# Performance work log

Measured on AMD Instinct MI355X. Metric: run time of the kernel, lower is better.

Reference implementation:

```python
import jax, jax.numpy as jnp
import numpy as np

B, D_IN, N = 128, 1024, 1024  # batch, input feature dim, output_dim


def setup_inputs() -> dict:
    key = jax.random.key(0)
    k1, k2, k3 = jax.random.split(key, 3)
    des = jax.random.normal(k1, (B, D_IN), dtype=jnp.float32)
    body = jax.random.normal(k2, (B, D_IN), dtype=jnp.float32)
    # keras 'uniform' initializer: RandomUniform(-0.05, 0.05)
    kernel = jax.random.uniform(k3, (D_IN, N), dtype=jnp.float32,
                                minval=-0.05, maxval=0.05)
    return {"des": des, "body": body, "kernel": kernel}


def _circulant_matvec(v, u):
    # Faithful to circulant(v) @ u from the original layer:
    # circ[b, k, j] = v[b, (k - j) mod n]  (column j of the circulant matrix is
    # v rolled down by j), then batch_dot over j -> circular convolution.
    n = v.shape[1]
    i = jnp.arange(n)
    idx = (i[:, None] - i[None, :]) % n        # (n, n) gather indices
    circ = v[:, idx]                           # (B, n, n)
    return jnp.einsum('bkj,bj->bk', circ, u)   # (B, n)


def reference(des, body, kernel):
    d = des @ kernel    # (B, N)
    b = body @ kernel   # (B, N)
    mv1 = _circulant_matvec(b, d)  # batch_dot(circulant(body'), des')
    mv2 = _circulant_matvec(d, b)  # batch_dot(circulant(des'), body')
    # Note: original computes K.dot(sum_vector, kernel) into sum_vector_1 but
    # returns sum_vector, so that dead op is omitted.
    return mv1 + mv2
```

## Files before the change

### kernel.cpp

```cpp
#include <hip/hip_runtime.h>


using bf16x8 = __attribute__((ext_vector_type(8))) short;
using f32x4  = __attribute__((ext_vector_type(4))) float;

static __device__ __forceinline__ unsigned cvt_pk_bf16(float lo, float hi) {
    unsigned r;
    asm("v_cvt_pk_bf16_f32 %0, %1, %2" : "=v"(r) : "v"(lo), "v"(hi));
    return r;
}

__global__ __launch_bounds__(512) void gemm_kernel(
    const float* __restrict__ des, const float* __restrict__ body,
    const float* __restrict__ kmat, float* __restrict__ P)
{
    __shared__ float smem[9216];
    short* Bl = (short*)smem;
    float* Rbuf = smem;

    const int tid = threadIdx.x;
    const int bid = blockIdx.x;
    const int rt = bid >> 5;
    const int ct = bid & 31;
    const int R0 = rt * 32, C0 = ct * 32;
    const float* Arow = (R0 < 128) ? (des + (size_t)R0 * 1024)
                                   : (body + (size_t)(R0 - 128) * 1024);

    const int lane = tid & 63;
    const int w = tid >> 6;
    const int lr = lane & 15;
    const int lk = lane >> 4;

    f32x4 acc[2][2];
    #pragma unroll
    for (int q = 0; q < 2; ++q)
        #pragma unroll
        for (int g = 0; g < 2; ++g) acc[q][g] = (f32x4){0.f, 0.f, 0.f, 0.f};

    #pragma unroll 1
    for (int round = 0; round < 2; ++round) {
        const int kb = round * 512;
        #pragma unroll
        for (int i = 0; i < 4; ++i) {
            int t4 = tid + i * 512;
            int ke2 = t4 >> 3, c4 = t4 & 7;
            int k = ke2 * 2;
            const float* src = kmat + (size_t)(kb + k) * 1024 + C0 + c4 * 4;
            float4 Fa = *(const float4*)src;
            float4 Fb = *(const float4*)(src + 1024);
            const float fa[4] = {Fa.x, Fa.y, Fa.z, Fa.w};
            const float fb[4] = {Fb.x, Fb.y, Fb.z, Fb.w};
            int kg = (k >> 3) & 3, kc = k >> 5, sw = (k >> 3) & 7;
            #pragma unroll
            for (int u = 0; u < 4; ++u) {
                int c = c4 * 4 + u;
                int unit = (((c >> 4) * 16 + kc) << 6) + (kg << 4) + ((c & 15) ^ sw);
                *(unsigned*)&Bl[unit * 8 + (k & 7)] = cvt_pk_bf16(fa[u], fb[u]);
            }
        }
        __syncthreads();

        #pragma unroll
        for (int s = 0; s < 2; ++s) {
            const int kc = w * 2 + s;
            const int kglob = kb + kc * 32 + lk * 8;

            bf16x8 afr[2];
            #pragma unroll
            for (int q = 0; q < 2; ++q) {
                const float* ap = Arow + (size_t)(q * 16 + lr) * 1024 + kglob;
                float4 F0 = *(const float4*)ap;
                float4 F1 = *(const float4*)(ap + 4);
                uint4 ua;
                ua.x = cvt_pk_bf16(F0.x, F0.y);
                ua.y = cvt_pk_bf16(F0.z, F0.w);
                ua.z = cvt_pk_bf16(F1.x, F1.y);
                ua.w = cvt_pk_bf16(F1.z, F1.w);
                afr[q] = *(bf16x8*)&ua;
            }
            const int slot = lr ^ ((kc * 4 + lk) & 7);
            #pragma unroll
            for (int g = 0; g < 2; ++g) {
                int unit = ((g * 16 + kc) << 6) + (lk << 4) + slot;
                bf16x8 bfr = *(const bf16x8*)&Bl[unit * 8];
                acc[0][g] = __builtin_amdgcn_mfma_f32_16x16x32_bf16(bfr, afr[0], acc[0][g], 0, 0, 0);
                acc[1][g] = __builtin_amdgcn_mfma_f32_16x16x32_bf16(bfr, afr[1], acc[1][g], 0, 0, 0);
            }
        }
        __syncthreads();
    }

    #pragma unroll
    for (int q = 0; q < 2; ++q)
        #pragma unroll
        for (int g = 0; g < 2; ++g) {
            int r = q * 16 + lr;
            int c = g * 16 + (lk << 2);
            *(f32x4*)&Rbuf[w * 1152 + r * 36 + c] = acc[q][g];
        }
    __syncthreads();
    {
        int o = tid * 2;
        int r = o >> 5, c = o & 31;
        float2 s = make_float2(0.f, 0.f);
        #pragma unroll
        for (int u = 0; u < 8; ++u) {
            float2 v = *(const float2*)&Rbuf[u * 1152 + r * 36 + c];
            s.x += v.x; s.y += v.y;
        }
        *(float2*)(P + (size_t)(R0 + r) * 1024 + C0 + c) = s;
    }
}

__global__ __launch_bounds__(256) void conv_kernel(
    const float* __restrict__ P, float* __restrict__ out)
{
    __shared__ float dl[1024];
    __shared__ float bl[1024];
    __shared__ float red[2304];

    const int tid = threadIdx.x;
    const int bid = blockIdx.x;
    const int r = bid >> 1;
    const int h = bid & 1;

    {
        int sw = tid ^ ((tid >> 3) & 7);
        ((float4*)dl)[sw]  = ((const float4*)(P + (size_t)r * 1024))[tid];
        ((float4*)bl)[tid] = ((const float4*)(P + (size_t)(128 + r) * 1024))[tid];
    }
    __syncthreads();

    const int jq = tid >> 6;
    const int t  = tid & 63;
    const int k0 = (h * 512 + t * 8 - jq * 256) & 1023;

#define RD(fidx) (((const float4*)dl)[(((fidx) >> 2) ^ ((((fidx) >> 2) >> 3) & 7))])

    float acc[8] = {0.f, 0.f, 0.f, 0.f, 0.f, 0.f, 0.f, 0.f};
    float4 A  = RD(k0);
    float4 Bv = RD((k0 + 4) & 1023);

    const float* bq = bl + jq * 256;
    #pragma unroll 4
    for (int jc = 0; jc < 256; jc += 4) {
        float4 bv = *(const float4*)&bq[jc];
        float4 Nv = RD((k0 - jc - 4) & 1023);
        acc[0] += bv.x * A.x;  acc[1] += bv.x * A.y;  acc[2] += bv.x * A.z;  acc[3] += bv.x * A.w;
        acc[4] += bv.x * Bv.x; acc[5] += bv.x * Bv.y; acc[6] += bv.x * Bv.z; acc[7] += bv.x * Bv.w;
        acc[0] += bv.y * Nv.w; acc[1] += bv.y * A.x;  acc[2] += bv.y * A.y;  acc[3] += bv.y * A.z;
        acc[4] += bv.y * A.w;  acc[5] += bv.y * Bv.x; acc[6] += bv.y * Bv.y; acc[7] += bv.y * Bv.z;
        acc[0] += bv.z * Nv.z; acc[1] += bv.z * Nv.w; acc[2] += bv.z * A.x;  acc[3] += bv.z * A.y;
        acc[4] += bv.z * A.z;  acc[5] += bv.z * A.w;  acc[6] += bv.z * Bv.x; acc[7] += bv.z * Bv.y;
        acc[0] += bv.w * Nv.y; acc[1] += bv.w * Nv.z; acc[2] += bv.w * Nv.w; acc[3] += bv.w * A.x;
        acc[4] += bv.w * A.y;  acc[5] += bv.w * A.z;  acc[6] += bv.w * A.w;  acc[7] += bv.w * Bv.x;
        Bv = A; A = Nv;
    }
#undef RD

    {
        float* rd = red + jq * 576 + t * 9;
        #pragma unroll
        for (int q = 0; q < 8; ++q) rd[q] = acc[q];
    }
    __syncthreads();
    {
        int t2 = tid >> 2, qb = (tid & 3) * 2;
        float s0 = 0.f, s1 = 0.f;
        #pragma unroll
        for (int u = 0; u < 4; ++u) {
            s0 += red[u * 576 + t2 * 9 + qb];
            s1 += red[u * 576 + t2 * 9 + qb + 1];
        }
        *(float2*)(out + (size_t)r * 1024 + h * 512 + tid * 2) =
            make_float2(2.f * s0, 2.f * s1);
    }
}

extern "C" void kernel_launch(void* const* d_in, const int* in_sizes, int n_in,
                              void* d_out, int out_size, void* d_ws, size_t ws_size,
                              hipStream_t stream) {
    const float* des  = (const float*)d_in[0];
    const float* body = (const float*)d_in[1];
    const float* kmat = (const float*)d_in[2];
    float* P = (float*)d_ws;

    gemm_kernel<<<256, 512, 0, stream>>>(des, body, kmat, P);
    conv_kernel<<<256, 256, 0, stream>>>(P, (float*)d_out);
}
```

Baseline: 20.06 us.

## Split GEMM over K into two partial buffers and widen conv blocks

The GEMM grid doubles to 512 blocks, with each block handling half of K (512) in a single round, and each half writes its own partial result buffer. The conv kernel sums the two partials while loading into shared memory. Conv blocks grow to 512 threads, each covering 128 of the j range, and an 8-way reduction follows. The aim is more parallelism and occupancy on a GPU with many CUs, at the cost of twice the intermediate writes and reads plus a larger shared reduction.

Measured after the change: 17.74 us, median of 2. -11.6%, faster.

```diff
diff --git a/kernel.cpp b/kernel.cpp
--- a/kernel.cpp
+++ b/kernel.cpp
@@ -12,7 +12,7 @@
 
 __global__ __launch_bounds__(512) void gemm_kernel(
     const float* __restrict__ des, const float* __restrict__ body,
-    const float* __restrict__ kmat, float* __restrict__ P)
+    const float* __restrict__ kmat, float* __restrict__ Ppart)
 {
     __shared__ float smem[9216];
     short* Bl = (short*)smem;
@@ -20,9 +20,11 @@
 
     const int tid = threadIdx.x;
     const int bid = blockIdx.x;
-    const int rt = bid >> 5;
-    const int ct = bid & 31;
+    const int kh = bid & 1;
+    const int ct = (bid >> 1) & 31;
+    const int rt = bid >> 6;
     const int R0 = rt * 32, C0 = ct * 32;
+    const int kb = kh * 512;
     const float* Arow = (R0 < 128) ? (des + (size_t)R0 * 1024)
                                    : (body + (size_t)(R0 - 128) * 1024);
 
@@ -37,58 +39,54 @@
         #pragma unroll
         for (int g = 0; g < 2; ++g) acc[q][g] = (f32x4){0.f, 0.f, 0.f, 0.f};
 
-    #pragma unroll 1
-    for (int round = 0; round < 2; ++round) {
-        const int kb = round * 512;
+    #pragma unroll
+    for (int i = 0; i < 4; ++i) {
+        int t4 = tid + i * 512;
+        int ke2 = t4 >> 3, c4 = t4 & 7;
+        int k = ke2 * 2;
+        const float* src = kmat + (size_t)(kb + k) * 1024 + C0 + c4 * 4;
+        float4 Fa = *(const float4*)src;
+        float4 Fb = *(const float4*)(src + 1024);
+        const float fa[4] = {Fa.x, Fa.y, Fa.z, Fa.w};
+        const float fb[4] = {Fb.x, Fb.y, Fb.z, Fb.w};
+        int kg = (k >> 3) & 3, kc = k >> 5, sw = (k >> 3) & 7;
         #pragma unroll
-        for (int i = 0; i < 4; ++i) {
-            int t4 = tid + i * 512;
-            int ke2 = t4 >> 3, c4 = t4 & 7;
-            int k = ke2 * 2;
-            const float* src = kmat + (size_t)(kb + k) * 1024 + C0 + c4 * 4;
-            float4 Fa = *(const float4*)src;
-            float4 Fb = *(const float4*)(src + 1024);
-            const float fa[4] = {Fa.x, Fa.y, Fa.z, Fa.w};
-            const float fb[4] = {Fb.x, Fb.y, Fb.z, Fb.w};
-            int kg = (k >> 3) & 3, kc = k >> 5, sw = (k >> 3) & 7;
-            #pragma unroll
-            for (int u = 0; u < 4; ++u) {
-                int c = c4 * 4 + u;
-                int unit = (((c >> 4) * 16 + kc) << 6) + (kg << 4) + ((c & 15) ^ sw);
-                *(unsigned*)&Bl[unit * 8 + (k & 7)] = cvt_pk_bf16(fa[u], fb[u]);
-            }
+        for (int u = 0; u < 4; ++u) {
+            int c = c4 * 4 + u;
+            int unit = (((c >> 4) * 16 + kc) << 6) + (kg << 4) + ((c & 15) ^ sw);
+            *(unsigned*)&Bl[unit * 8 + (k & 7)] = cvt_pk_bf16(fa[u], fb[u]);
         }
-        __syncthreads();
+    }
+    __syncthreads();
 
+    #pragma unroll
+    for (int s = 0; s < 2; ++s) {
+        const int kc = w * 2 + s;
+        const int kglob = kb + kc * 32 + lk * 8;
+
+        bf16x8 afr[2];
         #pragma unroll
-        for (int s = 0; s < 2; ++s) {
-            const int kc = w * 2 + s;
-            const int kglob = kb + kc * 32 + lk * 8;
-
-            bf16x8 afr[2];
-            #pragma unroll
-            for (int q = 0; q < 2; ++q) {
-                const float* ap = Arow + (size_t)(q * 16 + lr) * 1024 + kglob;
-                float4 F0 = *(const float4*)ap;
-                float4 F1 = *(const float4*)(ap + 4);
-                uint4 ua;
-                ua.x = cvt_pk_bf16(F0.x, F0.y);
-                ua.y = cvt_pk_bf16(F0.z, F0.w);
-                ua.z = cvt_pk_bf16(F1.x, F1.y);
-                ua.w = cvt_pk_bf16(F1.z, F1.w);
-                afr[q] = *(bf16x8*)&ua;
-            }
-            const int slot = lr ^ ((kc * 4 + lk) & 7);
-            #pragma unroll
-            for (int g = 0; g < 2; ++g) {
-                int unit = ((g * 16 + kc) << 6) + (lk << 4) + slot;
-                bf16x8 bfr = *(const bf16x8*)&Bl[unit * 8];
-                acc[0][g] = __builtin_amdgcn_mfma_f32_16x16x32_bf16(bfr, afr[0], acc[0][g], 0, 0, 0);
-                acc[1][g] = __builtin_amdgcn_mfma_f32_16x16x32_bf16(bfr, afr[1], acc[1][g], 0, 0, 0);
-            }
+        for (int q = 0; q < 2; ++q) {
+            const float* ap = Arow + (size_t)(q * 16 + lr) * 1024 + kglob;
+            float4 F0 = *(const float4*)ap;
+            float4 F1 = *(const float4*)(ap + 4);
+            uint4 ua;
+            ua.x = cvt_pk_bf16(F0.x, F0.y);
+            ua.y = cvt_pk_bf16(F0.z, F0.w);
+            ua.z = cvt_pk_bf16(F1.x, F1.y);
+            ua.w = cvt_pk_bf16(F1.z, F1.w);
+            afr[q] = *(bf16x8*)&ua;
         }
-        __syncthreads();
+        const int slot = lr ^ ((kc * 4 + lk) & 7);
+        #pragma unroll
+        for (int g = 0; g < 2; ++g) {
+            int unit = ((g * 16 + kc) << 6) + (lk << 4) + slot;
+            bf16x8 bfr = *(const bf16x8*)&Bl[unit * 8];
+            acc[0][g] = __builtin_amdgcn_mfma_f32_16x16x32_bf16(bfr, afr[0], acc[0][g], 0, 0, 0);
+            acc[1][g] = __builtin_amdgcn_mfma_f32_16x16x32_bf16(bfr, afr[1], acc[1][g], 0, 0, 0);
+        }
     }
+    __syncthreads();
 
     #pragma unroll
     for (int q = 0; q < 2; ++q)
@@ -108,16 +106,16 @@
             float2 v = *(const float2*)&Rbuf[u * 1152 + r * 36 + c];
             s.x += v.x; s.y += v.y;
         }
-        *(float2*)(P + (size_t)(R0 + r) * 1024 + C0 + c) = s;
+        *(float2*)(Ppart + (size_t)kh * 262144 + (size_t)(R0 + r) * 1024 + C0 + c) = s;
     }
 }
 
-__global__ __launch_bounds__(256) void conv_kernel(
-    const float* __restrict__ P, float* __restrict__ out)
+__global__ __launch_bounds__(512) void conv_kernel(
+    const float* __restrict__ Ppart, float* __restrict__ out)
 {
     __shared__ float dl[1024];
     __shared__ float bl[1024];
-    __shared__ float red[2304];
+    __shared__ float red[4608];
 
     const int tid = threadIdx.x;
     const int bid = blockIdx.x;
@@ -125,15 +123,19 @@
     const int h = bid & 1;
 
     {
-        int sw = tid ^ ((tid >> 3) & 7);
-        ((float4*)dl)[sw]  = ((const float4*)(P + (size_t)r * 1024))[tid];
-        ((float4*)bl)[tid] = ((const float4*)(P + (size_t)(128 + r) * 1024))[tid];
+        int isB = tid >> 8, i4 = tid & 255;
+        const float4* s0 = (const float4*)(Ppart + (size_t)(isB ? 128 + r : r) * 1024);
+        const float4* s1 = (const float4*)(Ppart + 262144 + (size_t)(isB ? 128 + r : r) * 1024);
+        float4 a = s0[i4], b = s1[i4];
+        float4 v = make_float4(a.x + b.x, a.y + b.y, a.z + b.z, a.w + b.w);
+        if (isB) ((float4*)bl)[i4] = v;
+        else     ((float4*)dl)[i4 ^ ((i4 >> 3) & 7)] = v;
     }
     __syncthreads();
 
-    const int jq = tid >> 6;
+    const int jo = tid >> 6;
     const int t  = tid & 63;
-    const int k0 = (h * 512 + t * 8 - jq * 256) & 1023;
+    const int k0 = (h * 512 + t * 8 - jo * 128) & 1023;
 
 #define RD(fidx) (((const float4*)dl)[(((fidx) >> 2) ^ ((((fidx) >> 2) >> 3) & 7))])
 
@@ -141,9 +143,9 @@
     float4 A  = RD(k0);
     float4 Bv = RD((k0 + 4) & 1023);
 
-    const float* bq = bl + jq * 256;
+    const float* bq = bl + jo * 128;
     #pragma unroll 4
-    for (int jc = 0; jc < 256; jc += 4) {
+    for (int jc = 0; jc < 128; jc += 4) {
         float4 bv = *(const float4*)&bq[jc];
         float4 Nv = RD((k0 - jc - 4) & 1023);
         acc[0] += bv.x * A.x;  acc[1] += bv.x * A.y;  acc[2] += bv.x * A.z;  acc[3] += bv.x * A.w;
@@ -159,21 +161,17 @@
 #undef RD
 
     {
-        float* rd = red + jq * 576 + t * 9;
+        float* rd = red + jo * 576 + t * 9;
         #pragma unroll
         for (int q = 0; q < 8; ++q) rd[q] = acc[q];
     }
     __syncthreads();
     {
-        int t2 = tid >> 2, qb = (tid & 3) * 2;
-        float s0 = 0.f, s1 = 0.f;
+        int tt = tid >> 3, qq = tid & 7;
+        float s = 0.f;
         #pragma unroll
-        for (int u = 0; u < 4; ++u) {
-            s0 += red[u * 576 + t2 * 9 + qb];
-            s1 += red[u * 576 + t2 * 9 + qb + 1];
-        }
-        *(float2*)(out + (size_t)r * 1024 + h * 512 + tid * 2) =
-            make_float2(2.f * s0, 2.f * s1);
+        for (int u = 0; u < 8; ++u) s += red[u * 576 + tt * 9 + qq];
+        out[(size_t)r * 1024 + h * 512 + tid] = 2.f * s;
     }
 }
 
@@ -183,8 +181,8 @@
     const float* des  = (const float*)d_in[0];
     const float* body = (const float*)d_in[1];
     const float* kmat = (const float*)d_in[2];
-    float* P = (float*)d_ws;
+    float* Ppart = (float*)d_ws;
 
-    gemm_kernel<<<256, 512, 0, stream>>>(des, body, kmat, P);
-    conv_kernel<<<256, 256, 0, stream>>>(P, (float*)d_out);
+    gemm_kernel<<<512, 512, 0, stream>>>(des, body, kmat, Ppart);
+    conv_kernel<<<256, 512, 0, stream>>>(Ppart, (float*)d_out);
 }
```
